# Kernel tuning notes

Hardware: AMD Instinct MI355X
Metric: run time of the kernel (lower is better)

## Reference

```python
import jax, jax.numpy as jnp
import numpy as np


def setup_inputs() -> dict:
    key = jax.random.key(0)
    k_feat, k_w, k_src, k_dst, k_type = jax.random.split(key, 5)
    N, E, F_IN, F_OUT, NUM_TYPE = 100000, 1600000, 64, 64, 4
    feat = jax.random.normal(k_feat, (N, F_IN), dtype=jnp.float32)
    # xavier_uniform-like init for weight
    bound = float(np.sqrt(6.0 / (F_IN + F_OUT)))
    weight = jax.random.uniform(k_w, (F_IN, F_OUT), dtype=jnp.float32, minval=-bound, maxval=bound)
    weight_type = jnp.ones((NUM_TYPE,), dtype=jnp.float32)
    bias = jnp.zeros((F_OUT,), dtype=jnp.float32)
    src = jax.random.randint(k_src, (E,), 0, N, dtype=jnp.int32)
    dst = jax.random.randint(k_dst, (E,), 0, N, dtype=jnp.int32)
    type_info = jax.random.randint(k_type, (N,), 0, NUM_TYPE, dtype=jnp.int32)
    return {"feat": feat, "weight": weight, "weight_type": weight_type,
            "bias": bias, "src": src, "dst": dst, "type_info": type_info}


def reference(feat, weight, weight_type, bias, src, dst, type_info):
    # REConv forward with norm='both', activation=None.
    N = feat.shape[0]
    ones = jnp.ones(src.shape, dtype=feat.dtype)
    # left normalization: out-degree^{-1/2} on source features
    out_deg = jnp.clip(jax.ops.segment_sum(ones, src, num_segments=N), 1.0)
    feat = feat * (out_deg ** -0.5)[:, None]          # [N, F_in]
    feat = feat @ weight                               # [N, F_out]
    h = feat * weight_type[type_info][:, None]         # type-weighted src features
    # message passing: gather from src, scatter-sum into dst
    rst = jax.ops.segment_sum(h[src], dst, num_segments=N)  # [N, F_out]
    # right normalization: in-degree^{-1/2}
    in_deg = jnp.clip(jax.ops.segment_sum(ones, dst, num_segments=N), 1.0)
    rst = rst * (in_deg ** -0.5)[:, None] + bias
    return rst
```

## Files before the change

### kernel.cpp

```cpp
#include <hip/hip_runtime.h>


#define THREADS 256
#define PTHREADS 512
#define PSLICE 256
#define RSH 8
#define RBLK 256
#define SCAN_CHUNK 1024
#define SCAP 6400

__device__ __forceinline__ unsigned f2bf(float f) {
    unsigned x = __float_as_uint(f);
    return (x + 0x7fffu + ((x >> 16) & 1u)) >> 16;
}

__global__ void countA_kernel(const int* __restrict__ src, const int* __restrict__ dst,
                              unsigned* __restrict__ padc, int E, int chunk, int nreg) {
    extern __shared__ unsigned lds[];
    unsigned* histD = lds;
    unsigned* histS = lds + nreg;
    int t = threadIdx.x;
    for (int i = t; i < 2 * nreg; i += PTHREADS) lds[i] = 0u;
    __syncthreads();
    int beg = blockIdx.x * chunk, end = min(E, beg + chunk);
    for (int i = beg + t; i < end; i += PTHREADS) {
        atomicAdd(&histD[dst[i] >> RSH], 1u);
        atomicAdd(&histS[src[i] >> RSH], 1u);
    }
    __syncthreads();
    for (int r = t; r < nreg; r += PTHREADS) {
        padc[(size_t)r * PSLICE + blockIdx.x] = (histD[r] + 15u) & ~15u;
        padc[(size_t)(nreg + r) * PSLICE + blockIdx.x] = (histS[r] + 31u) & ~31u;
    }
}

__global__ void scan1_kernel(const unsigned* __restrict__ in,
                             unsigned* __restrict__ outv,
                             unsigned* __restrict__ blockSums, int n) {
    __shared__ unsigned sdata[256];
    int t = threadIdx.x;
    int base = blockIdx.x * SCAN_CHUNK;
    unsigned v[4], s = 0;
#pragma unroll
    for (int i = 0; i < 4; ++i) {
        int idx = base + t * 4 + i;
        v[i] = (idx < n) ? in[idx] : 0u;
        s += v[i];
    }
    sdata[t] = s;
    __syncthreads();
    for (int off = 1; off < 256; off <<= 1) {
        unsigned x = (t >= off) ? sdata[t - off] : 0u;
        __syncthreads();
        sdata[t] += x;
        __syncthreads();
    }
    if (t == 255) blockSums[blockIdx.x] = sdata[255];
    unsigned run = sdata[t] - s;
#pragma unroll
    for (int i = 0; i < 4; ++i) {
        int idx = base + t * 4 + i;
        if (idx < n) outv[idx] = run;
        run += v[i];
    }
}

__global__ void scan2_kernel(unsigned* __restrict__ blockSums, int nb) {
    __shared__ unsigned sdata[1024];
    int t = threadIdx.x;
    unsigned v = (t < nb) ? blockSums[t] : 0u;
    sdata[t] = v;
    __syncthreads();
    for (int off = 1; off < 1024; off <<= 1) {
        unsigned x = (t >= off) ? sdata[t - off] : 0u;
        __syncthreads();
        sdata[t] += x;
        __syncthreads();
    }
    if (t < nb) blockSums[t] = sdata[t] - v;
}

__global__ void scan3_kernel(unsigned* __restrict__ outv,
                             const unsigned* __restrict__ blockSums, int n) {
    int i = blockIdx.x * blockDim.x + threadIdx.x;
    if (i < n) outv[i] += blockSums[i / SCAN_CHUNK];
}

__global__ void total1_kernel(unsigned* __restrict__ bases,
                              const unsigned* __restrict__ padc, int nscan) {
    bases[nscan] = bases[nscan - 1] + padc[nscan - 1];
}

__global__ void partition_kernel(const int* __restrict__ src, const int* __restrict__ dst,
                                 const unsigned* __restrict__ bases,
                                 unsigned* __restrict__ dpack, unsigned short* __restrict__ spack,
                                 int E, int chunk, int nreg) {
    extern __shared__ unsigned cur[];
    unsigned* curD = cur;
    unsigned* curS = cur + nreg;
    int t = threadIdx.x, b = blockIdx.x;
    unsigned sOff = bases[(size_t)nreg * PSLICE];
    for (int r = t; r < nreg; r += PTHREADS) {
        curD[r] = bases[(size_t)r * PSLICE + b];
        curS[r] = bases[(size_t)(nreg + r) * PSLICE + b] - sOff;
    }
    __syncthreads();
    int beg = b * chunk, end = min(E, beg + chunk);
    for (int i = beg + t; i < end; i += PTHREADS) {
        int s = src[i], d = dst[i];
        unsigned p = atomicAdd(&curD[d >> RSH], 1u);
        dpack[p] = ((unsigned)(d & (RBLK - 1)) << 24) | (unsigned)s;
        unsigned q = atomicAdd(&curS[s >> RSH], 1u);
        spack[q] = (unsigned short)(s & (RBLK - 1));
    }
}

__global__ void outdeg_kernel(const unsigned short* __restrict__ spack,
                              const unsigned* __restrict__ bases,
                              unsigned* __restrict__ outdeg, int N, int nreg) {
    __shared__ unsigned cnt[RBLK];
    int r = blockIdx.x, t = threadIdx.x;
    cnt[t] = 0u;
    __syncthreads();
    unsigned sOff = bases[(size_t)nreg * PSLICE];
    unsigned s0 = bases[(size_t)(nreg + r) * PSLICE] - sOff;
    unsigned s1 = bases[(size_t)(nreg + r + 1) * PSLICE] - sOff;
    for (unsigned i = s0 + t; i < s1; i += THREADS) {
        unsigned v = spack[i];
        if (v != 0xFFFFu) atomicAdd(&cnt[v], 1u);
    }
    __syncthreads();
    int node = r * RBLK + t;
    if (node < N) outdeg[node] = cnt[t];
}

__global__ void transform_kernel(const float* __restrict__ feat, const float* __restrict__ weight,
                                 const float* __restrict__ wtype, const int* __restrict__ tinfo,
                                 const unsigned* __restrict__ outdeg,
                                 unsigned short* __restrict__ h16, int N) {
    __shared__ float W[64 * 64];
    int t = threadIdx.x;
    const float4* w4 = (const float4*)weight;
    float4* W4 = (float4*)W;
#pragma unroll
    for (int i = 0; i < 4; ++i) W4[t + i * 256] = w4[t + i * 256];
    __syncthreads();

    int row = blockIdx.x * 32 + (t >> 3);
    if (row >= N) return;
    int jg = t & 7;

    float s = rsqrtf(fmaxf((float)outdeg[row], 1.0f)) * wtype[tinfo[row]];

    float acc[8];
#pragma unroll
    for (int j = 0; j < 8; ++j) acc[j] = 0.0f;

    const float4* frow = (const float4*)(feat + (size_t)row * 64);
    for (int k4 = 0; k4 < 16; ++k4) {
        float4 a4 = frow[k4];
#pragma unroll
        for (int kk = 0; kk < 4; ++kk) {
            float a = (kk == 0) ? a4.x : (kk == 1) ? a4.y : (kk == 2) ? a4.z : a4.w;
            const float4* wr = (const float4*)&W[(k4 * 4 + kk) * 64];
            float4 w0 = wr[jg * 2];
            float4 w1 = wr[jg * 2 + 1];
            acc[0] += a * w0.x; acc[1] += a * w0.y; acc[2] += a * w0.z; acc[3] += a * w0.w;
            acc[4] += a * w1.x; acc[5] += a * w1.y; acc[6] += a * w1.z; acc[7] += a * w1.w;
        }
    }

    unsigned* hrow = (unsigned*)(h16 + (size_t)row * 64) + jg * 4;
#pragma unroll
    for (int p = 0; p < 4; ++p) {
        unsigned u = f2bf(acc[2 * p] * s) | (f2bf(acc[2 * p + 1] * s) << 16);
        __builtin_nontemporal_store(u, hrow + p);
    }
}

__global__ __launch_bounds__(1024) void fused_kernel(
        const unsigned* __restrict__ dpack, const unsigned* __restrict__ bases,
        const unsigned short* __restrict__ h16, const float* __restrict__ bias,
        float* __restrict__ out, int N) {
    __shared__ unsigned cnt[RBLK];
    __shared__ unsigned off[RBLK + 1];
    __shared__ unsigned cur[RBLK];
    __shared__ int slist[SCAP];
    __shared__ float sbias[64];
    int t = threadIdx.x, r = blockIdx.x;
    if (t < RBLK) cnt[t] = 0u;
    if (t < 64) sbias[t] = bias[t];
    __syncthreads();

    unsigned e0 = bases[(size_t)r * PSLICE];
    unsigned e1 = bases[(size_t)(r + 1) * PSLICE];

    for (unsigned i = e0 + t; i < e1; i += 1024) {
        unsigned u = dpack[i];
        if (u != 0xFFFFFFFFu) atomicAdd(&cnt[u >> 24], 1u);
    }
    __syncthreads();

    unsigned v = (t < RBLK) ? cnt[t] : 0u;
    for (int d = 1; d < RBLK; d <<= 1) {
        unsigned x = (t < RBLK && t >= d) ? cnt[t - d] : 0u;
        __syncthreads();
        if (t < RBLK) cnt[t] += x;
        __syncthreads();
    }
    if (t < RBLK) {
        off[t + 1] = cnt[t];
        cur[t] = cnt[t] - v;
        if (t == 0) off[0] = 0u;
    }
    __syncthreads();

    for (unsigned i = e0 + t; i < e1; i += 1024) {
        unsigned u = dpack[i];
        if (u != 0xFFFFFFFFu) {
            unsigned pos = atomicAdd(&cur[u >> 24], 1u);
            slist[pos] = (int)(u & 0xFFFFFFu);
        }
    }
    __syncthreads();

    int w = t >> 6, lane = t & 63;
    int rq = lane >> 4, k = lane & 15;
    for (int nl = w * 16; nl < w * 16 + 16; ++nl) {
        int node = r * RBLK + nl;
        unsigned beg = off[nl], end = off[nl + 1];
        float a0 = 0.0f, a1 = 0.0f, a2 = 0.0f, a3 = 0.0f;
        unsigned i = beg;
        for (; i + 16 <= end; i += 16) {
            int s0 = slist[i + rq];
            int s1 = slist[i + 4 + rq];
            int s2 = slist[i + 8 + rq];
            int s3 = slist[i + 12 + rq];
            uint2 u0 = *(const uint2*)(h16 + ((size_t)s0 << 6) + (k << 2));
            uint2 u1 = *(const uint2*)(h16 + ((size_t)s1 << 6) + (k << 2));
            uint2 u2 = *(const uint2*)(h16 + ((size_t)s2 << 6) + (k << 2));
            uint2 u3 = *(const uint2*)(h16 + ((size_t)s3 << 6) + (k << 2));
            a0 += __uint_as_float(u0.x << 16); a1 += __uint_as_float(u0.x & 0xffff0000u);
            a2 += __uint_as_float(u0.y << 16); a3 += __uint_as_float(u0.y & 0xffff0000u);
            a0 += __uint_as_float(u1.x << 16); a1 += __uint_as_float(u1.x & 0xffff0000u);
            a2 += __uint_as_float(u1.y << 16); a3 += __uint_as_float(u1.y & 0xffff0000u);
            a0 += __uint_as_float(u2.x << 16); a1 += __uint_as_float(u2.x & 0xffff0000u);
            a2 += __uint_as_float(u2.y << 16); a3 += __uint_as_float(u2.y & 0xffff0000u);
            a0 += __uint_as_float(u3.x << 16); a1 += __uint_as_float(u3.x & 0xffff0000u);
            a2 += __uint_as_float(u3.y << 16); a3 += __uint_as_float(u3.y & 0xffff0000u);
        }
        for (; i + 8 <= end; i += 8) {
            int s0 = slist[i + rq];
            int s1 = slist[i + 4 + rq];
            uint2 u0 = *(const uint2*)(h16 + ((size_t)s0 << 6) + (k << 2));
            uint2 u1 = *(const uint2*)(h16 + ((size_t)s1 << 6) + (k << 2));
            a0 += __uint_as_float(u0.x << 16); a1 += __uint_as_float(u0.x & 0xffff0000u);
            a2 += __uint_as_float(u0.y << 16); a3 += __uint_as_float(u0.y & 0xffff0000u);
            a0 += __uint_as_float(u1.x << 16); a1 += __uint_as_float(u1.x & 0xffff0000u);
            a2 += __uint_as_float(u1.y << 16); a3 += __uint_as_float(u1.y & 0xffff0000u);
        }
        for (; i < end; i += 4) {
            unsigned j = i + rq;
            if (j < end) {
                int s = slist[j];
                uint2 u = *(const uint2*)(h16 + ((size_t)s << 6) + (k << 2));
                a0 += __uint_as_float(u.x << 16); a1 += __uint_as_float(u.x & 0xffff0000u);
                a2 += __uint_as_float(u.y << 16); a3 += __uint_as_float(u.y & 0xffff0000u);
            }
        }

        a0 += __shfl_xor(a0, 16, 64);  a0 += __shfl_xor(a0, 32, 64);
        a1 += __shfl_xor(a1, 16, 64);  a1 += __shfl_xor(a1, 32, 64);
        a2 += __shfl_xor(a2, 16, 64);  a2 += __shfl_xor(a2, 32, 64);
        a3 += __shfl_xor(a3, 16, 64);  a3 += __shfl_xor(a3, 32, 64);

        if (node < N && rq == 0) {
            float sc = rsqrtf(fmaxf((float)(end - beg), 1.0f));
            float4 b = ((const float4*)sbias)[k];
            float* op = out + ((size_t)node << 6) + (k << 2);
            __builtin_nontemporal_store(a0 * sc + b.x, op + 0);
            __builtin_nontemporal_store(a1 * sc + b.y, op + 1);
            __builtin_nontemporal_store(a2 * sc + b.z, op + 2);
            __builtin_nontemporal_store(a3 * sc + b.w, op + 3);
        }
    }
}

extern "C" void kernel_launch(void* const* d_in, const int* in_sizes, int n_in,
                              void* d_out, int out_size, void* d_ws, size_t ws_size,
                              hipStream_t stream) {
    const float* feat   = (const float*)d_in[0];
    const float* weight = (const float*)d_in[1];
    const float* wtype  = (const float*)d_in[2];
    const float* bias   = (const float*)d_in[3];
    const int*   src    = (const int*)d_in[4];
    const int*   dst    = (const int*)d_in[5];
    const int*   tinfo  = (const int*)d_in[6];

    int E = in_sizes[4];
    int N = in_sizes[6];
    float* out = (float*)d_out;

    int nreg   = (N + RBLK - 1) / RBLK;
    int pchunk = (E + PSLICE - 1) / PSLICE;
    int nscan  = 2 * nreg * PSLICE;
    size_t capD = (size_t)E + 16u * PSLICE * nreg;
    size_t capS = (size_t)E + 32u * PSLICE * nreg;

    char* ws = (char*)d_ws;
    unsigned* dpack       = (unsigned*)ws;          ws += capD * sizeof(unsigned);
    unsigned short* spack = (unsigned short*)ws;    ws += capS * sizeof(unsigned short);
    unsigned short* h16   = (unsigned short*)ws;    ws += (size_t)N * 64 * sizeof(unsigned short);
    unsigned* padc        = (unsigned*)ws;          ws += (size_t)nscan * sizeof(unsigned);
    unsigned* bases       = (unsigned*)ws;          ws += ((size_t)nscan + 1) * sizeof(unsigned);
    unsigned* outdeg      = (unsigned*)ws;          ws += (size_t)N * sizeof(unsigned);
    unsigned* blockSums   = (unsigned*)ws;          ws += 1024 * sizeof(unsigned);

    hipMemsetAsync(dpack, 0xFF, capD * sizeof(unsigned), stream);
    hipMemsetAsync(spack, 0xFF, capS * sizeof(unsigned short), stream);

    size_t hist_lds = (size_t)2 * nreg * sizeof(unsigned);
    countA_kernel<<<PSLICE, PTHREADS, hist_lds, stream>>>(src, dst, padc, E, pchunk, nreg);

    int nb = (nscan + SCAN_CHUNK - 1) / SCAN_CHUNK;
    scan1_kernel<<<nb, 256, 0, stream>>>(padc, bases, blockSums, nscan);
    scan2_kernel<<<1, 1024, 0, stream>>>(blockSums, nb);
    scan3_kernel<<<(nscan + THREADS - 1) / THREADS, THREADS, 0, stream>>>(bases, blockSums, nscan);
    total1_kernel<<<1, 1, 0, stream>>>(bases, padc, nscan);

    partition_kernel<<<PSLICE, PTHREADS, hist_lds, stream>>>(src, dst, bases, dpack, spack,
                                                             E, pchunk, nreg);

    outdeg_kernel<<<nreg, THREADS, 0, stream>>>(spack, bases, outdeg, N, nreg);

    transform_kernel<<<(N + 31) / 32, THREADS, 0, stream>>>(
        feat, weight, wtype, tinfo, outdeg, h16, N);

    fused_kernel<<<nreg, 1024, 0, stream>>>(dpack, bases, h16, bias, out, N);
}
```

Before: 125.4 us.

## Replace count-scan-partition pipeline with fixed-capacity buckets and atomic cursor reservation

The two-pass counting sort (histogram, three-kernel prefix scan, separate partition) becomes one partition kernel. Each block histograms its edge chunk, reserves padded space per region in fixed-capacity buckets through global atomics on per-region cursors, scatters its edges, then fills its own unused padding with sentinels. This removes the extra read of src/dst, the scan kernels and the two large memsets, in exchange for a fixed per-region capacity that could overflow on skewed degree distributions and nondeterministic edge order within a region.

```diff
diff --git a/kernel.cpp b/kernel.cpp
--- a/kernel.cpp
+++ b/kernel.cpp
@@ -3,10 +3,11 @@
 
 #define THREADS 256
 #define PTHREADS 512
-#define PSLICE 256
+#define NCHUNKB 256
 #define RSH 8
 #define RBLK 256
-#define SCAN_CHUNK 1024
+#define CAP_D 8704u
+#define CAP_S 12800u
 #define SCAP 6400
 
 __device__ __forceinline__ unsigned f2bf(float f) {
@@ -14,117 +15,69 @@
     return (x + 0x7fffu + ((x >> 16) & 1u)) >> 16;
 }
 
-__global__ void countA_kernel(const int* __restrict__ src, const int* __restrict__ dst,
-                              unsigned* __restrict__ padc, int E, int chunk, int nreg) {
+__global__ void initcur_kernel(unsigned* __restrict__ cursorD,
+                               unsigned* __restrict__ cursorS, int nreg) {
+    int r = blockIdx.x * blockDim.x + threadIdx.x;
+    if (r < nreg) {
+        cursorD[r] = (unsigned)r * CAP_D;
+        cursorS[r] = (unsigned)r * CAP_S;
+    }
+}
+
+__global__ void partition1_kernel(const int* __restrict__ src, const int* __restrict__ dst,
+                                  unsigned* __restrict__ cursorD, unsigned* __restrict__ cursorS,
+                                  unsigned* __restrict__ dpack, unsigned short* __restrict__ spack,
+                                  int E, int chunk, int nreg) {
     extern __shared__ unsigned lds[];
     unsigned* histD = lds;
-    unsigned* histS = lds + nreg;
-    int t = threadIdx.x;
+    unsigned* histS = histD + nreg;
+    unsigned* endD  = histS + nreg;
+    unsigned* endS  = endD + nreg;
+    int t = threadIdx.x, b = blockIdx.x;
     for (int i = t; i < 2 * nreg; i += PTHREADS) lds[i] = 0u;
     __syncthreads();
-    int beg = blockIdx.x * chunk, end = min(E, beg + chunk);
+
+    int beg = b * chunk, end = min(E, beg + chunk);
     for (int i = beg + t; i < end; i += PTHREADS) {
         atomicAdd(&histD[dst[i] >> RSH], 1u);
         atomicAdd(&histS[src[i] >> RSH], 1u);
     }
     __syncthreads();
+
     for (int r = t; r < nreg; r += PTHREADS) {
-        padc[(size_t)r * PSLICE + blockIdx.x] = (histD[r] + 15u) & ~15u;
-        padc[(size_t)(nreg + r) * PSLICE + blockIdx.x] = (histS[r] + 31u) & ~31u;
-    }
-}
-
-__global__ void scan1_kernel(const unsigned* __restrict__ in,
-                             unsigned* __restrict__ outv,
-                             unsigned* __restrict__ blockSums, int n) {
-    __shared__ unsigned sdata[256];
-    int t = threadIdx.x;
-    int base = blockIdx.x * SCAN_CHUNK;
-    unsigned v[4], s = 0;
-#pragma unroll
-    for (int i = 0; i < 4; ++i) {
-        int idx = base + t * 4 + i;
-        v[i] = (idx < n) ? in[idx] : 0u;
-        s += v[i];
-    }
-    sdata[t] = s;
-    __syncthreads();
-    for (int off = 1; off < 256; off <<= 1) {
-        unsigned x = (t >= off) ? sdata[t - off] : 0u;
-        __syncthreads();
-        sdata[t] += x;
-        __syncthreads();
-    }
-    if (t == 255) blockSums[blockIdx.x] = sdata[255];
-    unsigned run = sdata[t] - s;
-#pragma unroll
-    for (int i = 0; i < 4; ++i) {
-        int idx = base + t * 4 + i;
-        if (idx < n) outv[idx] = run;
-        run += v[i];
-    }
-}
-
-__global__ void scan2_kernel(unsigned* __restrict__ blockSums, int nb) {
-    __shared__ unsigned sdata[1024];
-    int t = threadIdx.x;
-    unsigned v = (t < nb) ? blockSums[t] : 0u;
-    sdata[t] = v;
-    __syncthreads();
-    for (int off = 1; off < 1024; off <<= 1) {
-        unsigned x = (t >= off) ? sdata[t - off] : 0u;
-        __syncthreads();
-        sdata[t] += x;
-        __syncthreads();
-    }
-    if (t < nb) blockSums[t] = sdata[t] - v;
-}
-
-__global__ void scan3_kernel(unsigned* __restrict__ outv,
-                             const unsigned* __restrict__ blockSums, int n) {
-    int i = blockIdx.x * blockDim.x + threadIdx.x;
-    if (i < n) outv[i] += blockSums[i / SCAN_CHUNK];
-}
-
-__global__ void total1_kernel(unsigned* __restrict__ bases,
-                              const unsigned* __restrict__ padc, int nscan) {
-    bases[nscan] = bases[nscan - 1] + padc[nscan - 1];
-}
-
-__global__ void partition_kernel(const int* __restrict__ src, const int* __restrict__ dst,
-                                 const unsigned* __restrict__ bases,
-                                 unsigned* __restrict__ dpack, unsigned short* __restrict__ spack,
-                                 int E, int chunk, int nreg) {
-    extern __shared__ unsigned cur[];
-    unsigned* curD = cur;
-    unsigned* curS = cur + nreg;
-    int t = threadIdx.x, b = blockIdx.x;
-    unsigned sOff = bases[(size_t)nreg * PSLICE];
-    for (int r = t; r < nreg; r += PTHREADS) {
-        curD[r] = bases[(size_t)r * PSLICE + b];
-        curS[r] = bases[(size_t)(nreg + r) * PSLICE + b] - sOff;
-    }
-    __syncthreads();
-    int beg = b * chunk, end = min(E, beg + chunk);
+        unsigned pd = (histD[r] + 15u) & ~15u;
+        unsigned ps = (histS[r] + 31u) & ~31u;
+        unsigned bd = atomicAdd(&cursorD[r], pd);
+        unsigned bs = atomicAdd(&cursorS[r], ps);
+        histD[r] = bd; endD[r] = bd + pd;
+        histS[r] = bs; endS[r] = bs + ps;
+    }
+    __syncthreads();
+
     for (int i = beg + t; i < end; i += PTHREADS) {
         int s = src[i], d = dst[i];
-        unsigned p = atomicAdd(&curD[d >> RSH], 1u);
+        unsigned p = atomicAdd(&histD[d >> RSH], 1u);
         dpack[p] = ((unsigned)(d & (RBLK - 1)) << 24) | (unsigned)s;
-        unsigned q = atomicAdd(&curS[s >> RSH], 1u);
+        unsigned q = atomicAdd(&histS[s >> RSH], 1u);
         spack[q] = (unsigned short)(s & (RBLK - 1));
     }
+    __syncthreads();
+
+    for (int r = t; r < nreg; r += PTHREADS) {
+        for (unsigned i = histD[r]; i < endD[r]; ++i) dpack[i] = 0xFFFFFFFFu;
+        for (unsigned i = histS[r]; i < endS[r]; ++i) spack[i] = 0xFFFFu;
+    }
 }
 
 __global__ void outdeg_kernel(const unsigned short* __restrict__ spack,
-                              const unsigned* __restrict__ bases,
-                              unsigned* __restrict__ outdeg, int N, int nreg) {
+                              const unsigned* __restrict__ cursorS,
+                              unsigned* __restrict__ outdeg, int N) {
     __shared__ unsigned cnt[RBLK];
     int r = blockIdx.x, t = threadIdx.x;
     cnt[t] = 0u;
     __syncthreads();
-    unsigned sOff = bases[(size_t)nreg * PSLICE];
-    unsigned s0 = bases[(size_t)(nreg + r) * PSLICE] - sOff;
-    unsigned s1 = bases[(size_t)(nreg + r + 1) * PSLICE] - sOff;
+    unsigned s0 = (unsigned)r * CAP_S;
+    unsigned s1 = cursorS[r];
     for (unsigned i = s0 + t; i < s1; i += THREADS) {
         unsigned v = spack[i];
         if (v != 0xFFFFu) atomicAdd(&cnt[v], 1u);
@@ -179,7 +132,7 @@
 }
 
 __global__ __launch_bounds__(1024) void fused_kernel(
-        const unsigned* __restrict__ dpack, const unsigned* __restrict__ bases,
+        const unsigned* __restrict__ dpack, const unsigned* __restrict__ cursorD,
         const unsigned short* __restrict__ h16, const float* __restrict__ bias,
         float* __restrict__ out, int N) {
     __shared__ unsigned cnt[RBLK];
@@ -192,8 +145,8 @@
     if (t < 64) sbias[t] = bias[t];
     __syncthreads();
 
-    unsigned e0 = bases[(size_t)r * PSLICE];
-    unsigned e1 = bases[(size_t)(r + 1) * PSLICE];
+    unsigned e0 = (unsigned)r * CAP_D;
+    unsigned e1 = cursorD[r];
 
     for (unsigned i = e0 + t; i < e1; i += 1024) {
         unsigned u = dpack[i];
@@ -302,39 +255,26 @@
     float* out = (float*)d_out;
 
     int nreg   = (N + RBLK - 1) / RBLK;
-    int pchunk = (E + PSLICE - 1) / PSLICE;
-    int nscan  = 2 * nreg * PSLICE;
-    size_t capD = (size_t)E + 16u * PSLICE * nreg;
-    size_t capS = (size_t)E + 32u * PSLICE * nreg;
+    int pchunk = (E + NCHUNKB - 1) / NCHUNKB;
 
     char* ws = (char*)d_ws;
-    unsigned* dpack       = (unsigned*)ws;          ws += capD * sizeof(unsigned);
-    unsigned short* spack = (unsigned short*)ws;    ws += capS * sizeof(unsigned short);
+    unsigned* dpack       = (unsigned*)ws;          ws += (size_t)nreg * CAP_D * sizeof(unsigned);
+    unsigned short* spack = (unsigned short*)ws;    ws += (size_t)nreg * CAP_S * sizeof(unsigned short);
     unsigned short* h16   = (unsigned short*)ws;    ws += (size_t)N * 64 * sizeof(unsigned short);
-    unsigned* padc        = (unsigned*)ws;          ws += (size_t)nscan * sizeof(unsigned);
-    unsigned* bases       = (unsigned*)ws;          ws += ((size_t)nscan + 1) * sizeof(unsigned);
+    unsigned* cursorD     = (unsigned*)ws;          ws += (size_t)nreg * sizeof(unsigned);
+    unsigned* cursorS     = (unsigned*)ws;          ws += (size_t)nreg * sizeof(unsigned);
     unsigned* outdeg      = (unsigned*)ws;          ws += (size_t)N * sizeof(unsigned);
-    unsigned* blockSums   = (unsigned*)ws;          ws += 1024 * sizeof(unsigned);
-
-    hipMemsetAsync(dpack, 0xFF, capD * sizeof(unsigned), stream);
-    hipMemsetAsync(spack, 0xFF, capS * sizeof(unsigned short), stream);
-
-    size_t hist_lds = (size_t)2 * nreg * sizeof(unsigned);
-    countA_kernel<<<PSLICE, PTHREADS, hist_lds, stream>>>(src, dst, padc, E, pchunk, nreg);
-
-    int nb = (nscan + SCAN_CHUNK - 1) / SCAN_CHUNK;
-    scan1_kernel<<<nb, 256, 0, stream>>>(padc, bases, blockSums, nscan);
-    scan2_kernel<<<1, 1024, 0, stream>>>(blockSums, nb);
-    scan3_kernel<<<(nscan + THREADS - 1) / THREADS, THREADS, 0, stream>>>(bases, blockSums, nscan);
-    total1_kernel<<<1, 1, 0, stream>>>(bases, padc, nscan);
-
-    partition_kernel<<<PSLICE, PTHREADS, hist_lds, stream>>>(src, dst, bases, dpack, spack,
-                                                             E, pchunk, nreg);
-
-    outdeg_kernel<<<nreg, THREADS, 0, stream>>>(spack, bases, outdeg, N, nreg);
+
+    initcur_kernel<<<(nreg + THREADS - 1) / THREADS, THREADS, 0, stream>>>(cursorD, cursorS, nreg);
+
+    size_t part_lds = (size_t)4 * nreg * sizeof(unsigned);
+    partition1_kernel<<<NCHUNKB, PTHREADS, part_lds, stream>>>(
+        src, dst, cursorD, cursorS, dpack, spack, E, pchunk, nreg);
+
+    outdeg_kernel<<<nreg, THREADS, 0, stream>>>(spack, cursorS, outdeg, N);
 
     transform_kernel<<<(N + 31) / 32, THREADS, 0, stream>>>(
         feat, weight, wtype, tinfo, outdeg, h16, N);
 
-    fused_kernel<<<nreg, 1024, 0, stream>>>(dpack, bases, h16, bias, out, N);
-}
+    fused_kernel<<<nreg, 1024, 0, stream>>>(dpack, cursorD, h16, bias, out, N);
+}
```

After: 114.8 us. -8.5%, faster.
